# Optimization experiments

Hardware: AMD Instinct MI355X
Metric: run time of the kernel (lower is better)

Reference implementation:

```python
import jax, jax.numpy as jnp
import numpy as np

S_IN, S_DIM, Z_DIM, PE_D = 22, 256, 128, 64
REGION_LENS = [("hd", 400), ("mhc", 300), ("pep", 15), ("lv", 110), ("lj", 50), ("hv", 100), ("hj", 48)]
L_TOTAL = 1 + sum(l for _, l in REGION_LENS)  # 1024 (collapse token + all regions)


def pos_encoding(idx, d=PE_D):
    # one_d: emb[p, i] = sin(p / 10000**(i/d)) if i even else cos(...)
    pos = idx.astype(jnp.float32)
    i = jnp.arange(d)
    inv_freq = jnp.power(jnp.float32(10000.0), -(i.astype(jnp.float32) / d))
    ang = pos[:, None] * inv_freq[None, :]
    return jnp.where((i % 2 == 0)[None, :], jnp.sin(ang), jnp.cos(ang))


def build_pair_id():
    # Vectorized equivalent of create_hierarchical_pairs for contiguous regions.
    lens = [1] + [l for _, l in REGION_LENS]
    ncond = len(REGION_LENS) - 1  # conditioning regions (all but hd)
    r = jnp.concatenate([jnp.full((l,), lab, dtype=jnp.int32) for lab, l in enumerate(lens)])
    pos = jnp.arange(L_TOTAL, dtype=jnp.int32)
    ri, rj = r[:, None], r[None, :]
    di = jnp.abs(pos[:, None] - pos[None, :])
    pid = jnp.zeros((L_TOTAL, L_TOTAL), dtype=jnp.int32)
    hdhd = (ri == 1) & (rj == 1)
    pid = jnp.where(hdhd & (di == 1), 2, pid)            # hd adjacent
    pid = jnp.where(hdhd & (di > 1), 3, pid)             # hd non-adjacent
    pid = jnp.where(((ri == 1) & (rj >= 2)) | ((rj == 1) & (ri >= 2)), 4, pid)  # hd-cond
    pid = jnp.where((ri == rj) & (ri >= 2), 3 + ri, pid)  # self cond region m -> 5+m
    m1 = jnp.minimum(ri, rj) - 2
    m2 = jnp.maximum(ri, rj) - 2
    cross = (ri >= 2) & (rj >= 2) & (ri != rj)
    pair_idx = m1 * ncond - m1 * (m1 + 1) // 2 + (m2 - m1 - 1)
    pid = jnp.where(cross, 5 + ncond + pair_idx, pid)    # cross cond pairs, counter order
    coll = (ri == 0) | (rj == 0)
    pid = jnp.where(coll & ~((ri == 0) & (rj == 0)), 1, pid)  # collapse row/col
    return jnp.clip(pid, 0, 31)


def setup_inputs() -> dict:
    key = jax.random.key(0)
    ki = iter(jax.random.split(key, 32))
    inp = {}
    for name, Lr in REGION_LENS:
        inp[name] = jax.random.uniform(next(ki), (Lr, S_IN), dtype=jnp.float32)
        inp[name + "_idx"] = jnp.arange(Lr, dtype=jnp.int32)
    inp["mask"] = jax.random.randint(next(ki), (400,), 0, 2).astype(jnp.int32)

    def xavier(k, fi, fo):
        lim = float(np.sqrt(6.0 / (fi + fo)))
        return jax.random.uniform(k, (fi, fo), minval=-lim, maxval=lim, dtype=jnp.float32)

    inp["W_seq"] = xavier(next(ki), S_IN, S_DIM); inp["b_seq"] = jnp.zeros((S_DIM,), jnp.float32)
    inp["W_pos"] = xavier(next(ki), PE_D, S_DIM); inp["b_pos"] = jnp.zeros((S_DIM,), jnp.float32)
    inp["W_p1"] = xavier(next(ki), 8, Z_DIM // 2); inp["b_p1"] = jnp.zeros((Z_DIM // 2,), jnp.float32)
    inp["W_p2"] = xavier(next(ki), 4, Z_DIM // 2); inp["b_p2"] = jnp.zeros((Z_DIM // 2,), jnp.float32)
    inp["collapse_token"] = jax.random.normal(next(ki), (1, S_DIM), dtype=jnp.float32) * 0.1
    inp["collapse_weight"] = jnp.ones((1,), jnp.float32)
    for name, _ in REGION_LENS:
        inp["rw_" + name] = jnp.ones((2,), jnp.float32)
    return inp


def reference(hd, mhc, pep, lv, lj, hv, hj,
              hd_idx, mhc_idx, pep_idx, lv_idx, lj_idx, hv_idx, hj_idx, mask,
              W_seq, b_seq, W_pos, b_pos, W_p1, b_p1, W_p2, b_p2,
              collapse_token, collapse_weight,
              rw_hd, rw_mhc, rw_pep, rw_lv, rw_lj, rw_hv, rw_hj):
    def region_s(aa, idx, rw):
        seq = aa @ W_seq + b_seq
        pos = pos_encoding(idx) @ W_pos + b_pos
        return rw[0] * seq + rw[1] * pos

    hd_m = jnp.where(mask[:, None] == 1, jnp.float32(0.0), hd)  # MASK token is the zero vector
    s_out = jnp.concatenate([
        collapse_weight * collapse_token,
        region_s(hd_m, hd_idx, rw_hd),
        region_s(mhc, mhc_idx, rw_mhc),
        region_s(pep, pep_idx, rw_pep),
        region_s(lv, lv_idx, rw_lv),
        region_s(lj, lj_idx, rw_lj),
        region_s(hv, hv_idx, rw_hv),
        region_s(hj, hj_idx, rw_hj),
    ], axis=0)  # (L_TOTAL, S_DIM)

    pid = build_pair_id()  # (L, L) int32, values in [0, 31]
    # one_hot(pid//4, 8) @ W_p1 + b_p1 == row gather; same math, same grads.
    z = jnp.concatenate([W_p1[pid // 4] + b_p1, W_p2[pid % 4] + b_p2], axis=-1)  # (L, L, Z_DIM)
    return s_out, z
```

## Files before the change

kernel.cpp:

```cpp
#include <hip/hip_runtime.h>
#include <hip/hip_bf16.h>
#include <math.h>

#define S_IN   22
#define S_DIM  256
#define PE_D   64
#define L_TOT  1024

__device__ __forceinline__ int region_of(int p) {
    return (p >= 1) + (p >= 401) + (p >= 701) + (p >= 716) +
           (p >= 826) + (p >= 876) + (p >= 976);
}

__global__ __launch_bounds__(256) void s_out_kernel(
    const float* __restrict__ hd,  const int* __restrict__ hd_idx,
    const float* __restrict__ mhc, const int* __restrict__ mhc_idx,
    const float* __restrict__ pep, const int* __restrict__ pep_idx,
    const float* __restrict__ lv,  const int* __restrict__ lv_idx,
    const float* __restrict__ lj,  const int* __restrict__ lj_idx,
    const float* __restrict__ hv,  const int* __restrict__ hv_idx,
    const float* __restrict__ hj,  const int* __restrict__ hj_idx,
    const int*  __restrict__ mask,
    const float* __restrict__ W_seq, const float* __restrict__ b_seq,
    const float* __restrict__ W_pos, const float* __restrict__ b_pos,
    const float* __restrict__ collapse_token,
    const float* __restrict__ collapse_weight,
    const float* __restrict__ rw_hd, const float* __restrict__ rw_mhc,
    const float* __restrict__ rw_pep, const float* __restrict__ rw_lv,
    const float* __restrict__ rw_lj, const float* __restrict__ rw_hv,
    const float* __restrict__ rw_hj,
    float* __restrict__ out)
{
    const int row = blockIdx.x;
    const int c   = threadIdx.x;

    if (row == 0) {
        out[c] = collapse_weight[0] * collapse_token[c];
        return;
    }

    const float* aa; const int* idx; const float* rw; int start; int isHd = 0;
    if      (row < 401) { aa = hd;  idx = hd_idx;  rw = rw_hd;  start = 1;   isHd = 1; }
    else if (row < 701) { aa = mhc; idx = mhc_idx; rw = rw_mhc; start = 401; }
    else if (row < 716) { aa = pep; idx = pep_idx; rw = rw_pep; start = 701; }
    else if (row < 826) { aa = lv;  idx = lv_idx;  rw = rw_lv;  start = 716; }
    else if (row < 876) { aa = lj;  idx = lj_idx;  rw = rw_lj;  start = 826; }
    else if (row < 976) { aa = hv;  idx = hv_idx;  rw = rw_hv;  start = 876; }
    else                { aa = hj;  idx = hj_idx;  rw = rw_hj;  start = 976; }
    const int r = row - start;

    __shared__ float sa[S_IN];
    __shared__ float pe[PE_D];

    if (c < S_IN) {
        float v = aa[r * S_IN + c];
        if (isHd && mask[r] == 1) v = 0.0f;
        sa[c] = v;
    }
    if (c >= 64 && c < 64 + PE_D) {
        const int d = c - 64;
        const float p = (float)idx[r];
        const float inv_freq = expf(-((float)d / (float)PE_D) * 9.210340371976184f);
        const float ang = p * inv_freq;
        pe[d] = (d & 1) ? cosf(ang) : sinf(ang);
    }
    __syncthreads();

    float acc_s = b_seq[c];
    #pragma unroll
    for (int f = 0; f < S_IN; ++f)
        acc_s = fmaf(sa[f], W_seq[f * S_DIM + c], acc_s);

    float acc_p = b_pos[c];
    #pragma unroll
    for (int d = 0; d < PE_D; ++d)
        acc_p = fmaf(pe[d], W_pos[d * S_DIM + c], acc_p);

    out[row * S_DIM + c] = rw[0] * acc_s + rw[1] * acc_p;
}

__global__ __launch_bounds__(256) void z_kernel(
    const float* __restrict__ W_p1, const float* __restrict__ b_p1,
    const float* __restrict__ W_p2, const float* __restrict__ b_p2,
    float4* __restrict__ z)
{
    __shared__ alignas(16) float table[26 * 128];
    for (int t = threadIdx.x; t < 26 * 128; t += 256) {
        const int p = t >> 7, k = t & 127;
        float v;
        if (k < 64) v = W_p1[(p >> 2) * 64 + k]       + b_p1[k];
        else        v = W_p2[(p & 3) * 64 + (k - 64)] + b_p2[k - 64];
        table[t] = v;
    }
    __syncthreads();

    const int total  = (L_TOT * L_TOT * 128) / 4;
    const int stride = gridDim.x * blockDim.x;
    for (int cidx = blockIdx.x * blockDim.x + threadIdx.x; cidx < total; cidx += stride) {
        const int pair = cidx >> 5;
        const int i = pair >> 10;
        const int j = pair & 1023;
        const int ri = region_of(i);
        const int rj = region_of(j);
        int pid;
        if (ri == 0 || rj == 0) {
            pid = (ri + rj == 0) ? 0 : 1;
        } else if (ri == 1 && rj == 1) {
            const int di = (i > j) ? (i - j) : (j - i);
            pid = (di == 1) ? 2 : ((di > 1) ? 3 : 0);
        } else if (ri == 1 || rj == 1) {
            pid = 4;
        } else if (ri == rj) {
            pid = 3 + ri;
        } else {
            const int m1 = ((ri < rj) ? ri : rj) - 2;
            const int m2 = ((ri > rj) ? ri : rj) - 2;
            pid = 11 + m1 * 6 - (m1 * (m1 + 1)) / 2 + (m2 - m1 - 1);
        }
        const int koff = cidx & 31;
        const float4* src =
            reinterpret_cast<const float4*>(&table[(pid << 7) + (koff << 2)]);
        z[cidx] = *src;
    }
}

extern "C" void kernel_launch(void* const* d_in, const int* in_sizes, int n_in,
                              void* d_out, int out_size, void* d_ws, size_t ws_size,
                              hipStream_t stream) {
    const float* hd       = (const float*)d_in[0];
    const int*   hd_idx   = (const int*)  d_in[1];
    const float* mhc      = (const float*)d_in[2];
    const int*   mhc_idx  = (const int*)  d_in[3];
    const float* pep      = (const float*)d_in[4];
    const int*   pep_idx  = (const int*)  d_in[5];
    const float* lv       = (const float*)d_in[6];
    const int*   lv_idx   = (const int*)  d_in[7];
    const float* lj       = (const float*)d_in[8];
    const int*   lj_idx   = (const int*)  d_in[9];
    const float* hv       = (const float*)d_in[10];
    const int*   hv_idx   = (const int*)  d_in[11];
    const float* hj       = (const float*)d_in[12];
    const int*   hj_idx   = (const int*)  d_in[13];
    const int*   mask     = (const int*)  d_in[14];
    const float* W_seq    = (const float*)d_in[15];
    const float* b_seq    = (const float*)d_in[16];
    const float* W_pos    = (const float*)d_in[17];
    const float* b_pos    = (const float*)d_in[18];
    const float* W_p1     = (const float*)d_in[19];
    const float* b_p1     = (const float*)d_in[20];
    const float* W_p2     = (const float*)d_in[21];
    const float* b_p2     = (const float*)d_in[22];
    const float* collapse_token  = (const float*)d_in[23];
    const float* collapse_weight = (const float*)d_in[24];
    const float* rw_hd    = (const float*)d_in[25];
    const float* rw_mhc   = (const float*)d_in[26];
    const float* rw_pep   = (const float*)d_in[27];
    const float* rw_lv    = (const float*)d_in[28];
    const float* rw_lj    = (const float*)d_in[29];
    const float* rw_hv    = (const float*)d_in[30];
    const float* rw_hj    = (const float*)d_in[31];

    float* out = (float*)d_out;

    s_out_kernel<<<L_TOT, 256, 0, stream>>>(
        hd, hd_idx, mhc, mhc_idx, pep, pep_idx, lv, lv_idx, lj, lj_idx,
        hv, hv_idx, hj, hj_idx, mask, W_seq, b_seq, W_pos, b_pos,
        collapse_token, collapse_weight,
        rw_hd, rw_mhc, rw_pep, rw_lv, rw_lj, rw_hv, rw_hj, out);

    z_kernel<<<8192, 256, 0, stream>>>(
        W_p1, b_p1, W_p2, b_p2,
        reinterpret_cast<float4*>(out + L_TOT * S_DIM));
}
```

Baseline: 601.4 us.

## Precompute per-row pair-id segments and stream z with nontemporal stores

The z kernel now gives each block one row i and a 256-wide j span. Thread 0 builds a small list of constant-pid j segments for that row, so the per-element region lookup and pid branching disappear from the inner loop. Stores become nontemporal float4 writes with one register value reused across each segment. The grid shrinks from 8192 to 4096 blocks. Segment iteration adds serial setup per block, and some segments give warps uneven work.

```diff
diff --git a/kernel.cpp b/kernel.cpp
--- a/kernel.cpp
+++ b/kernel.cpp
@@ -1,5 +1,4 @@
 #include <hip/hip_runtime.h>
-#include <hip/hip_bf16.h>
 #include <math.h>
 
 #define S_IN   22
@@ -7,10 +6,7 @@
 #define PE_D   64
 #define L_TOT  1024
 
-__device__ __forceinline__ int region_of(int p) {
-    return (p >= 1) + (p >= 401) + (p >= 701) + (p >= 716) +
-           (p >= 826) + (p >= 876) + (p >= 976);
-}
+typedef float f4 __attribute__((ext_vector_type(4)));
 
 __global__ __launch_bounds__(256) void s_out_kernel(
     const float* __restrict__ hd,  const int* __restrict__ hd_idx,
@@ -82,9 +78,12 @@
 __global__ __launch_bounds__(256) void z_kernel(
     const float* __restrict__ W_p1, const float* __restrict__ b_p1,
     const float* __restrict__ W_p2, const float* __restrict__ b_p2,
-    float4* __restrict__ z)
+    f4* __restrict__ z)
 {
     __shared__ alignas(16) float table[26 * 128];
+    __shared__ int seg_s[16], seg_e[16], seg_p[16];
+    __shared__ int ns_sh;
+
     for (int t = threadIdx.x; t < 26 * 128; t += 256) {
         const int p = t >> 7, k = t & 127;
         float v;
@@ -92,35 +91,62 @@
         else        v = W_p2[(p & 3) * 64 + (k - 64)] + b_p2[k - 64];
         table[t] = v;
     }
+
+    const int i  = blockIdx.x >> 2;
+    const int j0 = (blockIdx.x & 3) << 8;
+    const int j1 = j0 + 256;
+
+    if (threadIdx.x == 0) {
+        int ns = 0;
+        auto add = [&](int s, int e, int p) {
+            if (s < e) { seg_s[ns] = s; seg_e[ns] = e; seg_p[ns] = p; ++ns; }
+        };
+        const int ri = (i >= 1) + (i >= 401) + (i >= 701) + (i >= 716) +
+                       (i >= 826) + (i >= 876) + (i >= 976);
+        if (ri == 0) {
+            add(0, 1, 0);
+            add(1, L_TOT, 1);
+        } else {
+            const int rs[9] = {0, 1, 401, 701, 716, 826, 876, 976, 1024};
+            add(0, 1, 1);
+            #pragma unroll
+            for (int rj = 1; rj < 8; ++rj) {
+                const int s = rs[rj], e = rs[rj + 1];
+                if (ri == 1 && rj == 1) {
+                    add(1, i - 1, 3);
+                    add((i - 1 > 1 ? i - 1 : 1), i, 2);
+                    add(i, (i + 1 < 401 ? i + 1 : 401), 0);
+                    add(i + 1, (i + 2 < 401 ? i + 2 : 401), 2);
+                    add(i + 2, 401, 3);
+                } else if (ri == 1 || rj == 1) {
+                    add(s, e, 4);
+                } else if (ri == rj) {
+                    add(s, e, 3 + ri);
+                } else {
+                    const int m1 = ((ri < rj) ? ri : rj) - 2;
+                    const int m2 = ((ri > rj) ? ri : rj) - 2;
+                    add(s, e, 11 + m1 * 6 - (m1 * (m1 + 1)) / 2 + (m2 - m1 - 1));
+                }
+            }
+        }
+        ns_sh = ns;
+    }
     __syncthreads();
 
-    const int total  = (L_TOT * L_TOT * 128) / 4;
-    const int stride = gridDim.x * blockDim.x;
-    for (int cidx = blockIdx.x * blockDim.x + threadIdx.x; cidx < total; cidx += stride) {
-        const int pair = cidx >> 5;
-        const int i = pair >> 10;
-        const int j = pair & 1023;
-        const int ri = region_of(i);
-        const int rj = region_of(j);
-        int pid;
-        if (ri == 0 || rj == 0) {
-            pid = (ri + rj == 0) ? 0 : 1;
-        } else if (ri == 1 && rj == 1) {
-            const int di = (i > j) ? (i - j) : (j - i);
-            pid = (di == 1) ? 2 : ((di > 1) ? 3 : 0);
-        } else if (ri == 1 || rj == 1) {
-            pid = 4;
-        } else if (ri == rj) {
-            pid = 3 + ri;
-        } else {
-            const int m1 = ((ri < rj) ? ri : rj) - 2;
-            const int m2 = ((ri > rj) ? ri : rj) - 2;
-            pid = 11 + m1 * 6 - (m1 * (m1 + 1)) / 2 + (m2 - m1 - 1);
+    const int ns     = ns_sh;
+    const int koff   = threadIdx.x & 31;
+    const int lane_j = threadIdx.x >> 5;
+    f4* const zrow = z + ((size_t)i << 15);
+
+    for (int s = 0; s < ns; ++s) {
+        const int ss = seg_s[s], ee = seg_e[s];
+        const int js = ss > j0 ? ss : j0;
+        const int je = ee < j1 ? ee : j1;
+        if (js >= je) continue;
+        const f4 v = *reinterpret_cast<const f4*>(&table[(seg_p[s] << 7) + (koff << 2)]);
+        for (int j = js + lane_j; j < je; j += 8) {
+            __builtin_nontemporal_store(v, &zrow[(j << 5) + koff]);
         }
-        const int koff = cidx & 31;
-        const float4* src =
-            reinterpret_cast<const float4*>(&table[(pid << 7) + (koff << 2)]);
-        z[cidx] = *src;
     }
 }
 
@@ -168,7 +194,7 @@
         collapse_token, collapse_weight,
         rw_hd, rw_mhc, rw_pep, rw_lv, rw_lj, rw_hv, rw_hj, out);
 
-    z_kernel<<<8192, 256, 0, stream>>>(
+    z_kernel<<<4096, 256, 0, stream>>>(
         W_p1, b_p1, W_p2, b_p2,
-        reinterpret_cast<float4*>(out + L_TOT * S_DIM));
+        reinterpret_cast<f4*>(out + L_TOT * S_DIM));
 }
```

Result: no change. 597.0 us (-0.7%).
